# Optimization experiments

Measured on AMD Instinct MI355X. Metric: run time of the kernel, lower is better.

The kernel has to match this reference:

```python
import jax, jax.numpy as jnp
import numpy as np

N = 3000
NUM_CLASSES = 80
SIGMA = 0.5            # gaussian soft-NMS sigma (hardcoded 0.5 in forward)
SCORE_THRESHOLD = 0.05 # hardcoded 0.05 in forward


def setup_inputs() -> dict:
    key = jax.random.key(0)
    k1, k2, k3, k4 = jax.random.split(key, 4)
    # well-formed xyxy boxes: x2>x1, y2>y1
    xy = jax.random.uniform(k1, (N, 2), jnp.float32, 0.0, 1000.0)
    wh = jax.random.uniform(k2, (N, 2), jnp.float32, 10.0, 150.0)
    boxes = jnp.concatenate([xy, xy + wh], axis=1)          # [N,4]
    scores = jax.random.uniform(k3, (N,), jnp.float32)       # [N]
    idxs = jax.random.randint(k4, (N,), 0, NUM_CLASSES)      # [N] class ids
    return {"boxes": boxes, "scores": scores, "idxs": idxs}


def _iou_one_vs_all(box, boxes):
    # box [4], boxes [N,4] -> iou [N]
    x1 = jnp.maximum(box[0], boxes[:, 0])
    y1 = jnp.maximum(box[1], boxes[:, 1])
    x2 = jnp.minimum(box[2], boxes[:, 2])
    y2 = jnp.minimum(box[3], boxes[:, 3])
    inter = jnp.clip(x2 - x1, 0.0) * jnp.clip(y2 - y1, 0.0)
    area_a = (box[2] - box[0]) * (box[3] - box[1])
    area_b = (boxes[:, 2] - boxes[:, 0]) * (boxes[:, 3] - boxes[:, 1])
    return inter / (area_a + area_b - inter)


def _soft_nms(boxes, scores):
    # Sequential Gaussian soft-NMS. At step i: select remaining max-score box,
    # swap to slot i, decay all later scores by exp(-iou^2/sigma).
    n = boxes.shape[0]
    order = jnp.arange(n)
    rng = jnp.arange(n)

    def step(carry, i):
        b_s, s_s, ord_s = carry
        masked = jnp.where(rng < i, -jnp.inf, s_s)
        j = jnp.argmax(masked)
        # swap slots i and j in boxes / scores / order
        bi, bj = b_s[i], b_s[j]
        b_s = b_s.at[i].set(bj).at[j].set(bi)
        si, sj = s_s[i], s_s[j]
        s_s = s_s.at[i].set(sj).at[j].set(si)
        oi, oj = ord_s[i], ord_s[j]
        ord_s = ord_s.at[i].set(oj).at[j].set(oi)
        # gaussian decay of later boxes
        iou = _iou_one_vs_all(b_s[i], b_s)               # [N]
        decay = jnp.exp(-(iou * iou) / SIGMA)
        s_s = jnp.where(rng > i, s_s * decay, s_s)
        return (b_s, s_s, ord_s), None

    (b_s, s_s, ord_s), _ = jax.lax.scan(step, (boxes, scores, order), jnp.arange(n))
    return s_s, ord_s


def reference(boxes, scores, idxs):
    # batched trick: offset boxes per class so cross-class IoU is always 0
    max_coord = jnp.max(boxes)
    offsets = idxs.astype(boxes.dtype) * (max_coord + 1.0)   # [N]
    boxes_off = boxes + offsets[:, None]                     # [N,4]
    updated_scores, order = _soft_nms(boxes_off, scores)
    keep_mask = updated_scores > SCORE_THRESHOLD             # fixed-shape keep indicator
    return updated_scores, order, keep_mask
```

## Files before the change

kernel.cpp:

```cpp
#include <hip/hip_runtime.h>
#include <math.h>

#define NMAX 3008
#define NCH  47
#define CAPC 128
#define NCLS 80
#define TB   512
#define IC   6
#define JC   16
#define JCH  192
#define RB   (IC*JC)

#define WS_DONE   0
#define WS_FSCORE 16
#define WS_RANKC  (WS_FSCORE + 4*NMAX)

__device__ __forceinline__ float wave_max64(float x) {
    int v;
    v = __float_as_int(x);
    x = fmaxf(x, __int_as_float(__builtin_amdgcn_update_dpp(v, v, 0x111, 0xf, 0xf, false)));
    v = __float_as_int(x);
    x = fmaxf(x, __int_as_float(__builtin_amdgcn_update_dpp(v, v, 0x112, 0xf, 0xf, false)));
    v = __float_as_int(x);
    x = fmaxf(x, __int_as_float(__builtin_amdgcn_update_dpp(v, v, 0x114, 0xf, 0xf, false)));
    v = __float_as_int(x);
    x = fmaxf(x, __int_as_float(__builtin_amdgcn_update_dpp(v, v, 0x118, 0xf, 0xf, false)));
    v = __float_as_int(x);
    x = fmaxf(x, __int_as_float(__builtin_amdgcn_update_dpp(v, v, 0x142, 0xa, 0xf, false)));
    v = __float_as_int(x);
    x = fmaxf(x, __int_as_float(__builtin_amdgcn_update_dpp(v, v, 0x143, 0xc, 0xf, false)));
    return __int_as_float(__builtin_amdgcn_readlane(__float_as_int(x), 63));
}

__global__ void __launch_bounds__(TB)
nms_class_kernel(const float* __restrict__ boxes, const float* __restrict__ scores,
                 const int* __restrict__ idxs, char* __restrict__ ws, int n) {
#pragma clang fp contract(off)
    const int c = blockIdx.x;
    const int tid = threadIdx.x, wid = tid >> 6, lane = tid & 63;
    float* fscore = (float*)(ws + WS_FSCORE);
    unsigned long long* RANKC = (unsigned long long*)(ws + WS_RANKC);

    __shared__ unsigned long long maskS[NCH];
    __shared__ float mx0[CAPC], mx1[CAPC], mx2[CAPC], mx3[CAPC], msc[CAPC];
    __shared__ unsigned short mgid[CAPC];
    __shared__ float D[64 * 64];
    __shared__ unsigned long long ovMS[64];
    __shared__ float redS[TB / 64];

    for (int i = c * TB + tid; i < NMAX; i += NCLS * TB) RANKC[i] = 0ull;
    if (c == 0 && tid == 0) *(unsigned*)(ws + WS_DONE) = 0u;

    float m = -1e30f;
    for (int t = wid; t < NCH; t += 8) {
        int k = t * 64 + lane;
        bool p = false;
        if (k < n) {
            p = (idxs[k] == c);
            float4 bb = ((const float4*)boxes)[k];
            m = fmaxf(m, fmaxf(fmaxf(bb.x, bb.y), fmaxf(bb.z, bb.w)));
        }
        unsigned long long mk = __ballot(p);
        if (lane == 0) maskS[t] = mk;
    }
    m = wave_max64(m);
    if (lane == 0) redS[wid] = m;
    __syncthreads();
    float mm = redS[0];
#pragma unroll
    for (int w = 1; w < TB / 64; w++) mm = fmaxf(mm, redS[w]);
    const float maxcp1 = mm + 1.0f;
    const float off = (float)c * maxcp1;

    int run = 0;
    for (int t = 0; t < NCH; t++) {
        unsigned long long mk = maskS[t];
        if ((t & 7) == wid) {
            if ((mk >> lane) & 1ull) {
                int pos = run + __popcll(mk & ((1ull << lane) - 1ull));
                if (pos < CAPC) {
                    int k = t * 64 + lane;
                    float4 bb = ((const float4*)boxes)[k];
                    mx0[pos] = bb.x + off; mx1[pos] = bb.y + off;
                    mx2[pos] = bb.z + off; mx3[pos] = bb.w + off;
                    msc[pos] = scores[k];
                    mgid[pos] = (unsigned short)k;
                }
            }
        }
        run += __popcll(mk);
    }
    const int cnt = run < CAPC ? run : CAPC;
    __syncthreads();

    if (cnt <= 64) {
        const bool v0 = lane < cnt;
        float c0 = 0, c1 = 0, c2 = 0, c3 = 0;
        if (v0) { c0 = mx0[lane]; c1 = mx1[lane]; c2 = mx2[lane]; c3 = mx3[lane]; }
        const float ab = (c2 - c0) * (c3 - c1);
        for (int i = wid; i < cnt; i += 8) {
            float w0 = mx0[i], w1 = mx1[i], w2 = mx2[i], w3 = mx3[i];
            float aw = (w2 - w0) * (w3 - w1);
            float x1 = fmaxf(w0, c0), y1 = fmaxf(w1, c1);
            float x2 = fminf(w2, c2), y2 = fminf(w3, c3);
            float iw = fmaxf(x2 - x1, 0.f), ih = fmaxf(y2 - y1, 0.f);
            float inter = iw * ih;
            float d = 1.0f;
            if (inter != 0.f) {
                float iou = inter / ((aw + ab) - inter);
                float arg = -(iou * iou) / 0.5f;
                d = (float)exp((double)arg);
            }
            D[i * 64 + lane] = d;
            unsigned long long ov = __ballot(d != 1.0f);
            if (lane == 0) ovMS[i] = ov;
        }
        __syncthreads();

        if (wid == 0) {
            const bool v0b = lane < cnt;
            float sc = v0b ? msc[lane] : -1.f;
            int g = v0b ? mgid[lane] : 0;
            unsigned long long ovm = v0b ? (ovMS[lane] & ~(1ull << lane)) : 0ull;
            float frz = 0.f;
            for (;;) {
                unsigned long long rem = __ballot(sc >= 0.f);
                if (!rem) break;
                if (sc >= 0.f && (ovm & rem) == 0ull) { frz = sc; sc = -1.f; }
                rem = __ballot(sc >= 0.f);
                if (!rem) break;
                float M = wave_max64(sc);
                int wm = __ffsll(__ballot(sc == M)) - 1;
                float d = D[wm * 64 + lane];
                if (lane == wm) { frz = M; sc = -1.f; }
                else if (sc >= 0.f) sc = sc * d;
            }
            if (v0b) fscore[g] = frz;
        }
    } else if (wid == 0) {
        float sc0 = -1.f, sc1 = -1.f;
        float a0 = 0, a1 = 0, a2 = 0, a3 = 0, b0 = 0, b1 = 0, b2 = 0, b3 = 0;
        int g0 = 0, g1 = 0;
        if (lane < cnt) {
            sc0 = msc[lane];
            a0 = mx0[lane]; a1 = mx1[lane]; a2 = mx2[lane]; a3 = mx3[lane];
            g0 = mgid[lane];
        }
        if (64 + lane < cnt) {
            sc1 = msc[64 + lane];
            b0 = mx0[64 + lane]; b1 = mx1[64 + lane]; b2 = mx2[64 + lane]; b3 = mx3[64 + lane];
            g1 = mgid[64 + lane];
        }
        for (int s = 0; s < cnt; s++) {
            float M = fmaxf(sc0, sc1);
            for (int o = 32; o >= 1; o >>= 1) M = fmaxf(M, __shfl_xor(M, o, 64));
            unsigned long long balA = __ballot(sc0 == M);
            int wm;
            if (balA) wm = __ffsll(balA) - 1;
            else      wm = 64 + __ffsll(__ballot(sc1 == M)) - 1;
            float w0 = mx0[wm], w1 = mx1[wm], w2 = mx2[wm], w3 = mx3[wm];
            if (wm == lane)           { fscore[g0] = M; sc0 = -1.f; }
            else if (wm == 64 + lane) { fscore[g1] = M; sc1 = -1.f; }
            float area_w = (w2 - w0) * (w3 - w1);
            if (sc0 >= 0.f) {
                float x1 = fmaxf(w0, a0), y1 = fmaxf(w1, a1);
                float x2 = fminf(w2, a2), y2 = fminf(w3, a3);
                float iw = fmaxf(x2 - x1, 0.f), ih = fmaxf(y2 - y1, 0.f);
                float inter = iw * ih;
                float area_b = (a2 - a0) * (a3 - a1);
                float iou = inter / ((area_w + area_b) - inter);
                float arg = -(iou * iou) / 0.5f;
                sc0 = sc0 * (float)exp((double)arg);
            }
            if (sc1 >= 0.f) {
                float x1 = fmaxf(w0, b0), y1 = fmaxf(w1, b1);
                float x2 = fminf(w2, b2), y2 = fminf(w3, b3);
                float iw = fmaxf(x2 - x1, 0.f), ih = fmaxf(y2 - y1, 0.f);
                float inter = iw * ih;
                float area_b = (b2 - b0) * (b3 - b1);
                float iou = inter / ((area_w + area_b) - inter);
                float arg = -(iou * iou) / 0.5f;
                sc1 = sc1 * (float)exp((double)arg);
            }
        }
    }
}

__global__ void __launch_bounds__(TB)
rank_finalize_kernel(char* __restrict__ ws, float* __restrict__ out, int n) {
    const int tid = threadIdx.x;
    float* fscore = (float*)(ws + WS_FSCORE);
    unsigned long long* RANKC = (unsigned long long*)(ws + WS_RANKC);
    unsigned* done = (unsigned*)(ws + WS_DONE);

    __shared__ float sv[JCH];

    const int bx = blockIdx.x % IC;
    const int by = blockIdx.x / IC;
    const int chunk = (n + JC - 1) / JC;
    const int j0 = by * chunk;
    const int jn = min(n - j0, chunk);
    for (int j = tid; j < jn; j += TB) sv[j] = fscore[j0 + j];
    __syncthreads();

    int i = bx * TB + tid;
    if (i < n) {
        float s = fscore[i];
        int gt = 0, eq = 0, eqlt = 0;
        for (int jj = 0; jj < jn; jj++) {
            float x = sv[jj];
            gt   += (x > s) ? 1 : 0;
            eq   += (x == s) ? 1 : 0;
            eqlt += (x == s && (j0 + jj) < i) ? 1 : 0;
        }
        unsigned long long packed = (unsigned long long)(unsigned)gt
                                  | ((unsigned long long)(unsigned)eqlt << 16)
                                  | ((unsigned long long)(unsigned)eq << 32);
        atomicAdd(&RANKC[i], packed);
    }
    __syncthreads();
    __threadfence();

    __shared__ int lastS;
    if (tid == 0) lastS = (atomicAdd(done, 1u) == RB - 1);
    __syncthreads();
    if (!lastS) return;
    __threadfence();

    __shared__ unsigned short ordL[NMAX];
    __shared__ float          svL[NMAX];
    __shared__ unsigned short slotL[NMAX];
    __shared__ unsigned short batL[NMAX];
    __shared__ unsigned char  tieL[NMAX];
    __shared__ int rstopS;
    if (tid == 0) rstopS = 0;
    __syncthreads();

    for (int b = tid; b < n; b += TB) {
        unsigned long long p = __hip_atomic_load(&RANKC[b], __ATOMIC_RELAXED,
                                                 __HIP_MEMORY_SCOPE_AGENT);
        unsigned gt   = (unsigned)(p & 0xffffu);
        unsigned eqlt = (unsigned)((p >> 16) & 0xffffu);
        unsigned eq   = (unsigned)((p >> 32) & 0xffffu);
        int r = (int)(gt + eqlt);
        ordL[r] = (unsigned short)b;
        svL[r] = fscore[b];
        slotL[b] = (unsigned short)b;
        batL[b]  = (unsigned short)b;
        if (eq >= 2 && (unsigned)b < gt) atomicMax(&rstopS, (int)(gt + eq));
    }
    __syncthreads();

    for (int r = tid; r < n; r += TB)
        tieL[r] = (r + 1 < n) && (svL[r] == svL[r + 1]);
    __syncthreads();

    if (rstopS > 0 && tid == 0) {
        const int rstop = rstopS;
        int r = 0;
        while (r < rstop) {
            if (!tieL[r]) {
                int w = ordL[r];
                int j = slotL[w];
                int d = batL[r];
                batL[j] = (unsigned short)d;
                slotL[d] = (unsigned short)j;
                r++;
            } else {
                int g = 1;
                while (tieL[r + g - 1]) g++;
                for (int t = 0; t < g; t++) {
                    int bi = r + t;
                    int bs = slotL[ordL[bi]];
                    for (int q = r + t + 1; q < r + g; q++) {
                        int s2 = slotL[ordL[q]];
                        if (s2 < bs) { bs = s2; bi = q; }
                    }
                    unsigned short w = ordL[bi];
                    ordL[bi] = ordL[r + t];
                    ordL[r + t] = w;
                    int d = batL[r + t];
                    batL[bs] = (unsigned short)d;
                    slotL[d] = (unsigned short)bs;
                }
                r += g;
            }
        }
    }
    __syncthreads();

    for (int r = tid; r < n; r += TB) {
        float s = svL[r];
        out[r] = s;
        out[n + r] = (float)ordL[r];
        out[2 * n + r] = (s > 0.05f) ? 1.f : 0.f;
    }
}

extern "C" void kernel_launch(void* const* d_in, const int* in_sizes, int n_in,
                              void* d_out, int out_size, void* d_ws, size_t ws_size,
                              hipStream_t stream) {
    const float* boxes  = (const float*)d_in[0];
    const float* scores = (const float*)d_in[1];
    const int*   idxs   = (const int*)d_in[2];
    float* out = (float*)d_out;
    char* ws = (char*)d_ws;
    const int n = in_sizes[1];

    nms_class_kernel<<<NCLS, TB, 0, stream>>>(boxes, scores, idxs, ws, n);
    rank_finalize_kernel<<<RB, TB, 0, stream>>>(ws, out, n);
}
```

Before: 93.59 us.

## Split per-class soft-NMS into overlap components across waves; parallel prefix compaction

Replaces the serial per-chunk running count used for class compaction with a wave-level prefix scan over popcounts, so every wave can place its chunks independently. In the small-class path it labels connected components of the overlap graph by iterated min-label propagation in wave 0. Each component is then assigned to one of eight waves, so independent groups run their sequential soft-NMS loops concurrently instead of all in wave 0. This adds a label-propagation pass and an extra block barrier, and it relies on components not interacting, which holds because scores only decay through overlapping boxes.

```diff
diff --git a/kernel.cpp b/kernel.cpp
--- a/kernel.cpp
+++ b/kernel.cpp
@@ -46,6 +46,7 @@
     __shared__ unsigned short mgid[CAPC];
     __shared__ float D[64 * 64];
     __shared__ unsigned long long ovMS[64];
+    __shared__ int labS[64];
     __shared__ float redS[TB / 64];
 
     for (int i = c * TB + tid; i < NMAX; i += NCLS * TB) RANKC[i] = 0ull;
@@ -72,25 +73,31 @@
     const float maxcp1 = mm + 1.0f;
     const float off = (float)c * maxcp1;
 
-    int run = 0;
-    for (int t = 0; t < NCH; t++) {
+    int cS = (lane < NCH) ? __popcll(maskS[lane]) : 0;
+    int inc = cS;
+#pragma unroll
+    for (int o = 1; o < 64; o <<= 1) {
+        int y = __shfl_up(inc, o, 64);
+        if (lane >= o) inc += y;
+    }
+    const int baseEx = inc - cS;
+    const int total = __shfl(inc, NCH - 1, 64);
+    for (int t = wid; t < NCH; t += 8) {
         unsigned long long mk = maskS[t];
-        if ((t & 7) == wid) {
-            if ((mk >> lane) & 1ull) {
-                int pos = run + __popcll(mk & ((1ull << lane) - 1ull));
-                if (pos < CAPC) {
-                    int k = t * 64 + lane;
-                    float4 bb = ((const float4*)boxes)[k];
-                    mx0[pos] = bb.x + off; mx1[pos] = bb.y + off;
-                    mx2[pos] = bb.z + off; mx3[pos] = bb.w + off;
-                    msc[pos] = scores[k];
-                    mgid[pos] = (unsigned short)k;
-                }
-            }
-        }
-        run += __popcll(mk);
-    }
-    const int cnt = run < CAPC ? run : CAPC;
+        int bt = __shfl(baseEx, t, 64);
+        if ((mk >> lane) & 1ull) {
+            int pos = bt + __popcll(mk & ((1ull << lane) - 1ull));
+            if (pos < CAPC) {
+                int k = t * 64 + lane;
+                float4 bb = ((const float4*)boxes)[k];
+                mx0[pos] = bb.x + off; mx1[pos] = bb.y + off;
+                mx2[pos] = bb.z + off; mx3[pos] = bb.w + off;
+                msc[pos] = scores[k];
+                mgid[pos] = (unsigned short)k;
+            }
+        }
+    }
+    const int cnt = total < CAPC ? total : CAPC;
     __syncthreads();
 
     if (cnt <= 64) {
@@ -119,9 +126,36 @@
 
         if (wid == 0) {
             const bool v0b = lane < cnt;
-            float sc = v0b ? msc[lane] : -1.f;
-            int g = v0b ? mgid[lane] : 0;
             unsigned long long ovm = v0b ? (ovMS[lane] & ~(1ull << lane)) : 0ull;
+            int lab = lane;
+            if (ovm != 0ull) {
+                for (;;) {
+                    labS[lane] = lab;
+                    __asm__ volatile("s_waitcnt lgkmcnt(0)" ::: "memory");
+                    int mnew = lab;
+                    unsigned long long msk = ovm;
+                    while (msk) {
+                        int j = __ffsll(msk) - 1;
+                        msk &= msk - 1;
+                        int lj = labS[j];
+                        mnew = lj < mnew ? lj : mnew;
+                    }
+                    int lj2 = labS[mnew];
+                    mnew = lj2 < mnew ? lj2 : mnew;
+                    unsigned long long ch = __ballot(mnew != lab);
+                    lab = mnew;
+                    if (!ch) break;
+                }
+            }
+            labS[lane] = lab;
+        }
+        __syncthreads();
+
+        {
+            const bool mine = (lane < cnt) && ((labS[lane] & 7) == wid);
+            float sc = mine ? msc[lane] : -1.f;
+            int g = mine ? mgid[lane] : 0;
+            unsigned long long ovm = mine ? (ovMS[lane] & ~(1ull << lane)) : 0ull;
             float frz = 0.f;
             for (;;) {
                 unsigned long long rem = __ballot(sc >= 0.f);
@@ -135,7 +169,7 @@
                 if (lane == wm) { frz = M; sc = -1.f; }
                 else if (sc >= 0.f) sc = sc * d;
             }
-            if (v0b) fscore[g] = frz;
+            if (mine) fscore[g] = frz;
         }
     } else if (wid == 0) {
         float sc0 = -1.f, sc1 = -1.f;
```

Result: faster. 90.08 us (-3.7%).
